# Optimization experiments

Measured on AMD Instinct MI355X. Metric: run time of the kernel, lower is better.

Reference implementation:

```python
import jax, jax.numpy as jnp
import numpy as np

LORA_ALPHA = 32
LORA_RANK = 16
SCALING = LORA_ALPHA / LORA_RANK  # 2.0


def setup_inputs() -> dict:
    key = jax.random.key(0)
    ks = jax.random.split(key, 6)
    B_, S, D_IN, D_OUT, E, R = 4, 2048, 4096, 4096, 8, LORA_RANK
    x = jax.random.normal(ks[0], (B_, S, D_IN), dtype=jnp.float32)
    W_base = jax.random.normal(ks[1], (D_OUT, D_IN), dtype=jnp.float32) * (D_IN ** -0.5)
    b_base = jax.random.normal(ks[2], (D_OUT,), dtype=jnp.float32) * 0.01
    W_gate = jax.random.normal(ks[3], (E, D_IN), dtype=jnp.float32) * (D_IN ** -0.5)
    A = jax.random.normal(ks[4], (E, R, D_IN), dtype=jnp.float32) * (D_IN ** -0.5)
    B = jax.random.normal(ks[5], (D_OUT, R), dtype=jnp.float32)[None] * jnp.ones((E, 1, 1), jnp.float32) * 0.02
    B = jax.random.normal(ks[5], (E, D_OUT, R), dtype=jnp.float32) * 0.02
    return {"x": x, "W_base": W_base, "b_base": b_base, "W_gate": W_gate, "A": A, "B": B}


def reference(x, W_base, b_base, W_gate, A, B):
    # Base linear: [b,s,d_in] @ [d_out,d_in]^T -> [b,s,d_out]
    result = jnp.einsum('bsd,od->bso', x, W_base) + b_base
    # Softmax gating over experts: [b,s,E]
    route = jax.nn.softmax(jnp.einsum('bsd,ed->bse', x, W_gate), axis=-1)
    # All-expert low-rank down-projection: [b,s,E,r] (dropout is Identity, p=0)
    h = jnp.einsum('bsd,erd->bser', x, A)
    # Fuse route weight into the small low-rank intermediate before up-projection
    hw = h * route[..., None]
    # Weighted sum over experts of up-projection: [b,s,d_out]
    result = result + SCALING * jnp.einsum('bser,eor->bso', hw, B)
    return result
```

## Files before the change

### kernel.cpp

```cpp
#include <hip/hip_runtime.h>
#include <hip/hip_bf16.h>


typedef __attribute__((ext_vector_type(8))) short  bf16x8;
typedef __attribute__((ext_vector_type(4))) float  f32x4;
typedef __attribute__((ext_vector_type(4))) unsigned short us4;
typedef __attribute__((ext_vector_type(4))) float  fl4;

__device__ __forceinline__ unsigned short f2bf(float f) {
  unsigned int u = __float_as_uint(f);
  u += 0x7FFFu + ((u >> 16) & 1u);
  return (unsigned short)(u >> 16);
}
__device__ __forceinline__ float bf2f(unsigned short u) {
  return __uint_as_float(((unsigned int)u) << 16);
}
__device__ __forceinline__ void gload16(const void* g, void* l) {
  __builtin_amdgcn_global_load_lds(
      (const __attribute__((address_space(1))) unsigned int*)g,
      (__attribute__((address_space(3))) unsigned int*)l, 16, 0, 0);
}

#define BAR() do { asm volatile("" ::: "memory"); \
                   __builtin_amdgcn_s_barrier();  \
                   asm volatile("" ::: "memory"); } while (0)
#define VMCNT6() asm volatile("s_waitcnt vmcnt(6)" ::: "memory")
#define VMCNT0() asm volatile("s_waitcnt vmcnt(0)" ::: "memory")

#define WS_XBF 0u
#define WS_WBF 67108864u
#define WS_AG  100663296u
#define WS_U   101842944u
#define WS_HW  102891520u
#define WS_HP  104988672u

__global__ __launch_bounds__(256) void prep_kernel(
    const float* __restrict__ x, const float* __restrict__ Wb,
    const float* __restrict__ Wg, const float* __restrict__ A,
    const float* __restrict__ B,
    unsigned short* __restrict__ Xbf, unsigned short* __restrict__ Wbf,
    unsigned short* __restrict__ AG, unsigned short* __restrict__ U)
{
  const long N0 = 8388608;
  const long N1 = N0 + 4194304;
  const long N2 = N1 + 139264;
  const long N3 = N2 + 8192;
  const long N4 = N3 + 131072;
  long i = (long)blockIdx.x * blockDim.x + threadIdx.x;
  long stride = (long)gridDim.x * blockDim.x;
  for (; i < N4; i += stride) {
    if (i < N1) {
      const float* s; unsigned short* d; long j;
      if (i < N0) { s = x;  d = Xbf; j = i; }
      else        { s = Wb; d = Wbf; j = i - N0; }
      fl4 v = ((const fl4*)s)[j];
      us4 o; o[0]=f2bf(v[0]); o[1]=f2bf(v[1]); o[2]=f2bf(v[2]); o[3]=f2bf(v[3]);
      ((us4*)d)[j] = o;
    } else if (i < N2) {
      long j = i - N1;
      fl4 v = (j < 8192) ? ((const fl4*)Wg)[j] : ((const fl4*)A)[j - 8192];
      us4 o; o[0]=f2bf(v[0]); o[1]=f2bf(v[1]); o[2]=f2bf(v[2]); o[3]=f2bf(v[3]);
      ((us4*)AG)[j] = o;
    } else if (i < N3) {
      long j = i - N2;
      us4 z = (us4)0;
      ((us4*)(AG + 136*4096))[j] = z;
    } else {
      long j = i - N3;
      long o = j >> 5;
      long c4 = j & 31;
      long e = c4 >> 2, r4 = c4 & 3;
      fl4 v = ((const fl4*)B)[e*16384 + o*4 + r4];
      us4 t; t[0]=f2bf(2.f*v[0]); t[1]=f2bf(2.f*v[1]);
             t[2]=f2bf(2.f*v[2]); t[3]=f2bf(2.f*v[3]);
      ((us4*)U)[j] = t;
    }
  }
}

__global__ __launch_bounds__(256) void gate_partial(
    const unsigned short* __restrict__ Xbf,
    const unsigned short* __restrict__ AG,
    unsigned short* __restrict__ HP)
{
  __shared__ unsigned short Xt[32*32];
  __shared__ unsigned short At[160*32];

  int tid = threadIdx.x;
  int lane = tid & 63;
  int w = tid >> 6;
  int wm = w & 1, wn = w >> 1;
  int mt = blockIdx.x >> 1, ks = blockIdx.x & 1;
  long brow = (long)mt * 32;
  long kbase = (long)ks * 2048;

  f32x4 acc[5];
#pragma unroll
  for (int i = 0; i < 5; ++i) acc[i] = (f32x4){0.f,0.f,0.f,0.f};

  int r16 = lane & 15, kh = lane >> 4;

  for (int kb = 0; kb < 64; ++kb) {
    long kc = kbase + kb*32;
    __syncthreads();
    for (int s = w; s < 11; s += 4) {
      if (s < 2)
        gload16(Xbf + (brow + s*16 + (lane>>2))*4096 + kc + (lane&3)*8,
                (char*)Xt + s*1024);
      else
        gload16(AG + ((long)((s-2)*16 + (lane>>2)))*4096 + kc + (lane&3)*8,
                (char*)At + (s-2)*1024);
    }
    __syncthreads();
    bf16x8 a = *(const bf16x8*)&Xt[(wm*16 + r16)*32 + kh*8];
#pragma unroll
    for (int c = 0; c < 5; ++c) {
      int ch = wn*5 + c;
      bf16x8 b = *(const bf16x8*)&At[(ch*16 + r16)*32 + kh*8];
      acc[c] = __builtin_amdgcn_mfma_f32_16x16x32_bf16(a, b, acc[c], 0, 0, 0);
    }
  }

  long rowg = brow + wm*16 + (lane>>4)*4;
#pragma unroll
  for (int c = 0; c < 5; ++c) {
    int ch = wn*5 + c;
    if (ch > 8) continue;
    int col = ch*16 + r16;
    if (col < 136) {
#pragma unroll
      for (int j = 0; j < 4; ++j)
        HP[((long)ks*8192 + rowg + j)*136 + col] = f2bf(acc[c][j]);
    }
  }
}

__global__ __launch_bounds__(256) void gate_reduce(
    const unsigned short* __restrict__ HP,
    unsigned short* __restrict__ HW)
{
  int tid = threadIdx.x;
  long r = (long)blockIdx.x*64 + (tid>>2);
  int q = tid & 3;
  const us4* r0 = (const us4*)(HP + r*136);
  const us4* r1 = (const us4*)(HP + (8192 + r)*136);

  us4 la0 = r0[0], la1 = r0[1], lb0 = r1[0], lb1 = r1[1];
  float lg[8];
#pragma unroll
  for (int e = 0; e < 4; ++e) {
    lg[e]   = bf2f(la0[e]) + bf2f(lb0[e]);
    lg[4+e] = bf2f(la1[e]) + bf2f(lb1[e]);
  }
  float mx = lg[0];
#pragma unroll
  for (int e = 1; e < 8; ++e) mx = fmaxf(mx, lg[e]);
  float ex[8]; float s = 0.f;
#pragma unroll
  for (int e = 0; e < 8; ++e) { ex[e] = __expf(lg[e] - mx); s += ex[e]; }
  float inv = 1.f / s;

  us4* ow = (us4*)(HW + r*128);
#pragma unroll
  for (int k = 0; k < 8; ++k) {
    us4 h0 = r0[2 + q*8 + k], h1 = r1[2 + q*8 + k];
    int col0 = q*32 + k*4;
    float rt = ex[col0 >> 4] * inv;
    us4 o;
#pragma unroll
    for (int i = 0; i < 4; ++i)
      o[i] = f2bf((bf2f(h0[i]) + bf2f(h1[i])) * rt);
    ow[q*8 + k] = o;
  }
}

#define NKT 66

struct Op { const unsigned short* a; const unsigned short* b; long lda, ldb, k0; };

__device__ __forceinline__ Op getop(int kt,
    const unsigned short* X, const unsigned short* W,
    const unsigned short* HW, const unsigned short* U) {
  Op o;
  if (kt < 64) { o.a = X;  o.b = W; o.lda = 4096; o.ldb = 4096; o.k0 = (long)kt*64; }
  else         { o.a = HW; o.b = U; o.lda = 128;  o.ldb = 128;  o.k0 = (long)(kt-64)*64; }
  return o;
}

__device__ __forceinline__ void stA(const unsigned short* src, long ld, long k0,
                                    long brow, char* dst, int mh, int t) {
  int l = t & 63, w = t >> 6;
  int kc = ((l & 7) ^ (l >> 3)) << 3;
#pragma unroll
  for (int i = 0; i < 2; ++i) {
    long grow = (long)i*128 + mh*64 + w*8 + (l>>3);
    gload16(src + (brow + grow)*ld + k0 + kc,
            dst + mh*8192 + i*16384 + (long)t*16);
  }
}
__device__ __forceinline__ void stB(const unsigned short* src, long ld, long k0,
                                    long bcol, char* dst, int nh, int t) {
  int l = t & 63, w = t >> 6;
  int kc = ((l & 7) ^ (l >> 3)) << 3;
#pragma unroll
  for (int i = 0; i < 2; ++i) {
    long grow = ((long)i*2 + (w>>2))*64 + nh*32 + (w&3)*8 + (l>>3);
    gload16(src + (bcol + grow)*ld + k0 + kc,
            dst + i*16384 + (w>>2)*8192 + nh*4096 + ((long)(w&3)*64 + l)*16);
  }
}

__device__ __forceinline__ bf16x8 frag(const char* buf, int row, int ks, int kh, int l7) {
  int slot = (ks*4 + kh) ^ l7;
  return *(const bf16x8*)(buf + (long)row*128 + slot*16);
}

__global__ __launch_bounds__(512, 2) void gemm8(
    const unsigned short* __restrict__ Xbf,
    const unsigned short* __restrict__ Wbf,
    const unsigned short* __restrict__ HW,
    const unsigned short* __restrict__ U,
    const float* __restrict__ bias,
    float* __restrict__ out)
{
  __shared__ char lds[131072];

  int tid = threadIdx.x;
  int lane = tid & 63;
  int w = tid >> 6;
  int wr = w >> 2, wc = w & 3;
  int r16 = lane & 15, kh = lane >> 4, l7 = lane & 7;

  int bid = blockIdx.x;
  long brow = (long)(bid >> 4) * 256;
  long bcol = (long)(bid & 15) * 256;

  f32x4 acc[2][2][4][2];
#pragma unroll
  for (int mh = 0; mh < 2; ++mh)
#pragma unroll
    for (int nh = 0; nh < 2; ++nh)
#pragma unroll
      for (int m = 0; m < 4; ++m)
#pragma unroll
        for (int n = 0; n < 2; ++n) acc[mh][nh][m][n] = (f32x4){0.f,0.f,0.f,0.f};

  char* A0b = lds;
  char* B0b = lds + 65536;

  {
    Op o0 = getop(0, Xbf, Wbf, HW, U);
    Op o1 = getop(1, Xbf, Wbf, HW, U);
    stA(o0.a, o0.lda, o0.k0, brow, A0b, 0, tid);
    stB(o0.b, o0.ldb, o0.k0, bcol, B0b, 0, tid);
    stB(o0.b, o0.ldb, o0.k0, bcol, B0b, 1, tid);
    stA(o0.a, o0.lda, o0.k0, brow, A0b, 1, tid);
    stA(o1.a, o1.lda, o1.k0, brow, A0b + 32768, 0, tid);
    stB(o1.b, o1.ldb, o1.k0, bcol, B0b + 32768, 0, tid);
    stB(o1.b, o1.ldb, o1.k0, bcol, B0b + 32768, 1, tid);
    VMCNT6();
    BAR();
  }

  bf16x8 a[4][2], b0[2][2], b1[2][2];

  for (int kt = 0; kt < NKT; ++kt) {
    const char* rA = A0b + (kt & 1) * 32768;
    const char* rB = B0b + (kt & 1) * 32768;
    char* wA1 = A0b + ((kt + 1) & 1) * 32768;
    char* wA2 = A0b + (kt & 1) * 32768;
    char* wB2 = B0b + (kt & 1) * 32768;
    Op o1 = getop(kt + 1 < NKT ? kt + 1 : 0, Xbf, Wbf, HW, U);
    Op o2 = getop(kt + 2 < NKT ? kt + 2 : 0, Xbf, Wbf, HW, U);

#pragma unroll
    for (int m = 0; m < 4; ++m)
#pragma unroll
      for (int ks = 0; ks < 2; ++ks)
        a[m][ks] = frag(rA, wr*128 + m*16 + r16, ks, kh, l7);
#pragma unroll
    for (int n = 0; n < 2; ++n)
#pragma unroll
      for (int ks = 0; ks < 2; ++ks)
        b0[n][ks] = frag(rB, wc*64 + n*16 + r16, ks, kh, l7);
    if (kt + 1 < NKT) stA(o1.a, o1.lda, o1.k0, brow, wA1, 1, tid);
    BAR();
    __builtin_amdgcn_s_setprio(1);
#pragma unroll
    for (int m = 0; m < 4; ++m)
#pragma unroll
      for (int n = 0; n < 2; ++n)
#pragma unroll
        for (int ks = 0; ks < 2; ++ks)
          acc[0][0][m][n] = __builtin_amdgcn_mfma_f32_16x16x32_bf16(
              a[m][ks], b0[n][ks], acc[0][0][m][n], 0, 0, 0);
    __builtin_amdgcn_s_setprio(0);
    BAR();

#pragma unroll
    for (int n = 0; n < 2; ++n)
#pragma unroll
      for (int ks = 0; ks < 2; ++ks)
        b1[n][ks] = frag(rB, wc*64 + 32 + n*16 + r16, ks, kh, l7);
    if (kt + 2 < NKT) stA(o2.a, o2.lda, o2.k0, brow, wA2, 0, tid);
    BAR();
    __builtin_amdgcn_s_setprio(1);
#pragma unroll
    for (int m = 0; m < 4; ++m)
#pragma unroll
      for (int n = 0; n < 2; ++n)
#pragma unroll
        for (int ks = 0; ks < 2; ++ks)
          acc[0][1][m][n] = __builtin_amdgcn_mfma_f32_16x16x32_bf16(
              a[m][ks], b1[n][ks], acc[0][1][m][n], 0, 0, 0);
    __builtin_amdgcn_s_setprio(0);
    BAR();

#pragma unroll
    for (int m = 0; m < 4; ++m)
#pragma unroll
      for (int ks = 0; ks < 2; ++ks)
        a[m][ks] = frag(rA, wr*128 + 64 + m*16 + r16, ks, kh, l7);
    if (kt + 2 < NKT) stB(o2.b, o2.ldb, o2.k0, bcol, wB2, 0, tid);
    BAR();
    __builtin_amdgcn_s_setprio(1);
#pragma unroll
    for (int m = 0; m < 4; ++m)
#pragma unroll
      for (int n = 0; n < 2; ++n)
#pragma unroll
        for (int ks = 0; ks < 2; ++ks)
          acc[1][1][m][n] = __builtin_amdgcn_mfma_f32_16x16x32_bf16(
              a[m][ks], b1[n][ks], acc[1][1][m][n], 0, 0, 0);
    __builtin_amdgcn_s_setprio(0);
    BAR();

    if (kt + 2 < NKT) {
      stB(o2.b, o2.ldb, o2.k0, bcol, wB2, 1, tid);
      VMCNT6();
    } else if (kt + 1 < NKT) {
      VMCNT0();
    }
    BAR();
    __builtin_amdgcn_s_setprio(1);
#pragma unroll
    for (int m = 0; m < 4; ++m)
#pragma unroll
      for (int n = 0; n < 2; ++n)
#pragma unroll
        for (int ks = 0; ks < 2; ++ks)
          acc[1][0][m][n] = __builtin_amdgcn_mfma_f32_16x16x32_bf16(
              a[m][ks], b0[n][ks], acc[1][0][m][n], 0, 0, 0);
    __builtin_amdgcn_s_setprio(0);
    BAR();
  }

  int rg = lane >> 4;
#pragma unroll
  for (int mh = 0; mh < 2; ++mh)
#pragma unroll
    for (int nh = 0; nh < 2; ++nh)
#pragma unroll
      for (int n = 0; n < 2; ++n) {
        long col = bcol + wc*64 + nh*32 + n*16 + r16;
        float bv = bias[col];
#pragma unroll
        for (int m = 0; m < 4; ++m) {
          long row0 = brow + wr*128 + mh*64 + m*16 + rg*4;
#pragma unroll
          for (int j = 0; j < 4; ++j)
            out[(row0 + j)*4096 + col] = acc[mh][nh][m][n][j] + bv;
        }
      }
}

extern "C" void kernel_launch(void* const* d_in, const int* in_sizes, int n_in,
                              void* d_out, int out_size, void* d_ws, size_t ws_size,
                              hipStream_t stream) {
  (void)in_sizes; (void)n_in; (void)out_size; (void)ws_size;
  const float* x  = (const float*)d_in[0];
  const float* Wb = (const float*)d_in[1];
  const float* bb = (const float*)d_in[2];
  const float* Wg = (const float*)d_in[3];
  const float* A  = (const float*)d_in[4];
  const float* B  = (const float*)d_in[5];
  float* out = (float*)d_out;
  char* ws = (char*)d_ws;

  unsigned short* Xbf = (unsigned short*)(ws + WS_XBF);
  unsigned short* Wbf = (unsigned short*)(ws + WS_WBF);
  unsigned short* AG  = (unsigned short*)(ws + WS_AG);
  unsigned short* U   = (unsigned short*)(ws + WS_U);
  unsigned short* HW  = (unsigned short*)(ws + WS_HW);
  unsigned short* HP  = (unsigned short*)(ws + WS_HP);

  hipLaunchKernelGGL(prep_kernel, dim3(2048), dim3(256), 0, stream,
                     x, Wb, Wg, A, B, Xbf, Wbf, AG, U);
  hipLaunchKernelGGL(gate_partial, dim3(512), dim3(256), 0, stream,
                     Xbf, AG, HP);
  hipLaunchKernelGGL(gate_reduce, dim3(128), dim3(256), 0, stream,
                     HP, HW);
  hipLaunchKernelGGL(gemm8, dim3(512), dim3(512), 0, stream,
                     Xbf, Wbf, HW, U, bb, out);
}
```

Measured before the change: 564.2 us.

## Fuse gate projection, split-K reduce and softmax into one kernel; remap gemm blocks

Replaces the two-kernel gate path (split-K partial GEMM writing bf16 partials to workspace, then a reduce/softmax kernel) with one kernel. Each block handles 16 rows, the four waves split K and load operands straight from global memory into registers, and the partials are reduced in LDS before the softmax and route weighting. This removes one launch and the HP round trip through global memory, and keeps the partial sums in fp32 instead of rounding them to bf16. It also permutes the block index in the main GEMM so that co-scheduled blocks share tiles, for better L2 reuse. The risk is that direct global loads without LDS staging may be less efficient for the gate GEMM.

```diff
diff --git a/kernel.cpp b/kernel.cpp
--- a/kernel.cpp
+++ b/kernel.cpp
@@ -11,9 +11,6 @@
   unsigned int u = __float_as_uint(f);
   u += 0x7FFFu + ((u >> 16) & 1u);
   return (unsigned short)(u >> 16);
-}
-__device__ __forceinline__ float bf2f(unsigned short u) {
-  return __uint_as_float(((unsigned int)u) << 16);
 }
 __device__ __forceinline__ void gload16(const void* g, void* l) {
   __builtin_amdgcn_global_load_lds(
@@ -32,7 +29,6 @@
 #define WS_AG  100663296u
 #define WS_U   101842944u
 #define WS_HW  102891520u
-#define WS_HP  104988672u
 
 __global__ __launch_bounds__(256) void prep_kernel(
     const float* __restrict__ x, const float* __restrict__ Wb,
@@ -78,99 +74,69 @@
   }
 }
 
-__global__ __launch_bounds__(256) void gate_partial(
+__global__ __launch_bounds__(256, 2) void gate_fused(
     const unsigned short* __restrict__ Xbf,
     const unsigned short* __restrict__ AG,
-    unsigned short* __restrict__ HP)
+    unsigned short* __restrict__ HW)
 {
-  __shared__ unsigned short Xt[32*32];
-  __shared__ unsigned short At[160*32];
+  __shared__ float part[4][16][148];
 
   int tid = threadIdx.x;
   int lane = tid & 63;
   int w = tid >> 6;
-  int wm = w & 1, wn = w >> 1;
-  int mt = blockIdx.x >> 1, ks = blockIdx.x & 1;
-  long brow = (long)mt * 32;
-  long kbase = (long)ks * 2048;
-
-  f32x4 acc[5];
-#pragma unroll
-  for (int i = 0; i < 5; ++i) acc[i] = (f32x4){0.f,0.f,0.f,0.f};
-
+  long brow = (long)blockIdx.x * 16;
   int r16 = lane & 15, kh = lane >> 4;
 
-  for (int kb = 0; kb < 64; ++kb) {
-    long kc = kbase + kb*32;
-    __syncthreads();
-    for (int s = w; s < 11; s += 4) {
-      if (s < 2)
-        gload16(Xbf + (brow + s*16 + (lane>>2))*4096 + kc + (lane&3)*8,
-                (char*)Xt + s*1024);
-      else
-        gload16(AG + ((long)((s-2)*16 + (lane>>2)))*4096 + kc + (lane&3)*8,
-                (char*)At + (s-2)*1024);
-    }
-    __syncthreads();
-    bf16x8 a = *(const bf16x8*)&Xt[(wm*16 + r16)*32 + kh*8];
-#pragma unroll
-    for (int c = 0; c < 5; ++c) {
-      int ch = wn*5 + c;
-      bf16x8 b = *(const bf16x8*)&At[(ch*16 + r16)*32 + kh*8];
+  f32x4 acc[9];
+#pragma unroll
+  for (int i = 0; i < 9; ++i) acc[i] = (f32x4){0.f,0.f,0.f,0.f};
+
+  const long kw = (long)w * 1024;
+  const unsigned short* xp = Xbf + (brow + r16)*4096 + kw + kh*8;
+  const unsigned short* gp = AG + (long)r16*4096 + kw + kh*8;
+
+#pragma unroll 2
+  for (int ks = 0; ks < 32; ++ks) {
+    long k = (long)ks * 32;
+    bf16x8 a = *(const bf16x8*)(xp + k);
+#pragma unroll
+    for (int c = 0; c < 9; ++c) {
+      bf16x8 b = *(const bf16x8*)(gp + (long)c*16*4096 + k);
       acc[c] = __builtin_amdgcn_mfma_f32_16x16x32_bf16(a, b, acc[c], 0, 0, 0);
     }
   }
 
-  long rowg = brow + wm*16 + (lane>>4)*4;
-#pragma unroll
-  for (int c = 0; c < 5; ++c) {
-    int ch = wn*5 + c;
-    if (ch > 8) continue;
-    int col = ch*16 + r16;
-    if (col < 136) {
-#pragma unroll
-      for (int j = 0; j < 4; ++j)
-        HP[((long)ks*8192 + rowg + j)*136 + col] = f2bf(acc[c][j]);
+  int rg = lane >> 4;
+#pragma unroll
+  for (int c = 0; c < 9; ++c)
+#pragma unroll
+    for (int j = 0; j < 4; ++j)
+      part[w][rg*4 + j][c*16 + r16] = acc[c][j];
+  __syncthreads();
+
+  {
+    int r = tid >> 4;
+    int q = tid & 15;
+    float lg[8];
+#pragma unroll
+    for (int e = 0; e < 8; ++e)
+      lg[e] = part[0][r][e] + part[1][r][e] + part[2][r][e] + part[3][r][e];
+    float mx = lg[0];
+#pragma unroll
+    for (int e = 1; e < 8; ++e) mx = fmaxf(mx, lg[e]);
+    float ex[8]; float s = 0.f;
+#pragma unroll
+    for (int e = 0; e < 8; ++e) { ex[e] = __expf(lg[e] - mx); s += ex[e]; }
+    float rt = ex[q >> 1] / s;
+    int c0 = 8 + q*8;
+    bf16x8 o;
+#pragma unroll
+    for (int j = 0; j < 8; ++j) {
+      float hv = part[0][r][c0+j] + part[1][r][c0+j]
+               + part[2][r][c0+j] + part[3][r][c0+j];
+      o[j] = (short)f2bf(hv * rt);
     }
-  }
-}
-
-__global__ __launch_bounds__(256) void gate_reduce(
-    const unsigned short* __restrict__ HP,
-    unsigned short* __restrict__ HW)
-{
-  int tid = threadIdx.x;
-  long r = (long)blockIdx.x*64 + (tid>>2);
-  int q = tid & 3;
-  const us4* r0 = (const us4*)(HP + r*136);
-  const us4* r1 = (const us4*)(HP + (8192 + r)*136);
-
-  us4 la0 = r0[0], la1 = r0[1], lb0 = r1[0], lb1 = r1[1];
-  float lg[8];
-#pragma unroll
-  for (int e = 0; e < 4; ++e) {
-    lg[e]   = bf2f(la0[e]) + bf2f(lb0[e]);
-    lg[4+e] = bf2f(la1[e]) + bf2f(lb1[e]);
-  }
-  float mx = lg[0];
-#pragma unroll
-  for (int e = 1; e < 8; ++e) mx = fmaxf(mx, lg[e]);
-  float ex[8]; float s = 0.f;
-#pragma unroll
-  for (int e = 0; e < 8; ++e) { ex[e] = __expf(lg[e] - mx); s += ex[e]; }
-  float inv = 1.f / s;
-
-  us4* ow = (us4*)(HW + r*128);
-#pragma unroll
-  for (int k = 0; k < 8; ++k) {
-    us4 h0 = r0[2 + q*8 + k], h1 = r1[2 + q*8 + k];
-    int col0 = q*32 + k*4;
-    float rt = ex[col0 >> 4] * inv;
-    us4 o;
-#pragma unroll
-    for (int i = 0; i < 4; ++i)
-      o[i] = f2bf((bf2f(h0[i]) + bf2f(h1[i])) * rt);
-    ow[q*8 + k] = o;
+    *(bf16x8*)&HW[(brow + r)*128 + q*8] = o;
   }
 }
 
@@ -231,7 +197,7 @@
   int wr = w >> 2, wc = w & 3;
   int r16 = lane & 15, kh = lane >> 4, l7 = lane & 7;
 
-  int bid = blockIdx.x;
+  int bid = ((blockIdx.x & 7) << 6) + (blockIdx.x >> 3);
   long brow = (long)(bid >> 4) * 256;
   long bcol = (long)(bid & 15) * 256;
 
@@ -392,14 +358,11 @@
   unsigned short* AG  = (unsigned short*)(ws + WS_AG);
   unsigned short* U   = (unsigned short*)(ws + WS_U);
   unsigned short* HW  = (unsigned short*)(ws + WS_HW);
-  unsigned short* HP  = (unsigned short*)(ws + WS_HP);
 
   hipLaunchKernelGGL(prep_kernel, dim3(2048), dim3(256), 0, stream,
                      x, Wb, Wg, A, B, Xbf, Wbf, AG, U);
-  hipLaunchKernelGGL(gate_partial, dim3(512), dim3(256), 0, stream,
-                     Xbf, AG, HP);
-  hipLaunchKernelGGL(gate_reduce, dim3(128), dim3(256), 0, stream,
-                     HP, HW);
+  hipLaunchKernelGGL(gate_fused, dim3(512), dim3(256), 0, stream,
+                     Xbf, AG, HW);
   hipLaunchKernelGGL(gemm8, dim3(512), dim3(512), 0, stream,
                      Xbf, Wbf, HW, U, bb, out);
 }
```

Result: slower. 577.4 us (+2.3%).
